# Kernel optimization log

Measured on AMD Instinct MI355X. Metric: run time of the kernel, lower is better.

Reference implementation:

```python
import jax, jax.numpy as jnp
import numpy as np
import math

B, T, F, H = 8, 1024, 512, 8
D = F // H  # 64
MIN_VAL = float(np.finfo(np.float32).min)


def setup_inputs() -> dict:
    key = jax.random.key(0)
    ks = jax.random.split(key, 16)
    w = lambda k, shape: jax.random.normal(k, shape, dtype=jnp.float32) * 0.02
    return {
        "query": jax.random.normal(ks[0], (B, T, F), dtype=jnp.float32),
        "key": jax.random.normal(ks[1], (B, T, F), dtype=jnp.float32),
        "value": jax.random.normal(ks[2], (B, T, F), dtype=jnp.float32),
        "mask": jax.random.randint(ks[3], (B, T, T), 0, 2, dtype=jnp.int32),
        "pos_emb": jax.random.normal(ks[4], (1, T, F), dtype=jnp.float32),
        "Wq": w(ks[5], (F, F)), "bq": jnp.zeros((F,), jnp.float32),
        "Wk": w(ks[6], (F, F)), "bk": jnp.zeros((F,), jnp.float32),
        "Wv": w(ks[7], (F, F)), "bv": jnp.zeros((F,), jnp.float32),
        "Wp": w(ks[8], (F, F)),
        "Wo": w(ks[9], (F, F)), "bo": jnp.zeros((F,), jnp.float32),
        "pos_bias_u": w(ks[10], (H, D)),
        "pos_bias_v": w(ks[11], (H, D)),
    }


def reference(query, key, value, mask, pos_emb, Wq, bq, Wk, bk, Wv, bv, Wp, Wo, bo, pos_bias_u, pos_bias_v):
    n_batch = query.shape[0]
    # projections (torch Linear: x @ W.T + b)
    q = (query @ Wq.T + bq).reshape(n_batch, -1, H, D)          # (B, T1, H, D)
    k = (key @ Wk.T + bk).reshape(n_batch, -1, H, D).transpose(0, 2, 1, 3)    # (B, H, T2, D)
    v = (value @ Wv.T + bv).reshape(n_batch, -1, H, D).transpose(0, 2, 1, 3)  # (B, H, T2, D)
    # relative position projection; pos_emb batch is 1 -> squeeze for broadcast
    p = (pos_emb @ Wp.T).reshape(pos_emb.shape[0], -1, H, D).transpose(0, 2, 1, 3)[0]  # (H, T2, D)

    q_u = q + pos_bias_u  # broadcast (H, D) over (B, T1, H, D)
    q_v = q + pos_bias_v
    matrix_ac = jnp.einsum("bthd,bhsd->bhts", q_u, k)
    matrix_bd = jnp.einsum("bthd,hsd->bhts", q_v, p)
    scores = (matrix_ac + matrix_bd) / math.sqrt(D)  # (B, H, T1, T2)

    m = (mask[:, None, :, :] == 0)  # (B, 1, T1, T2)
    scores = jnp.where(m, MIN_VAL, scores)
    attn = jnp.where(m, 0.0, jax.nn.softmax(scores, axis=-1))

    x = jnp.einsum("bhts,bhsd->bthd", attn, v).reshape(n_batch, -1, H * D)
    return x @ Wo.T + bo
```

## Files before the change

### kernel.cpp

```cpp
#include <hip/hip_runtime.h>

typedef float f32x4 __attribute__((ext_vector_type(4)));
typedef short bf16x8 __attribute__((ext_vector_type(8)));
typedef unsigned short u16x8 __attribute__((ext_vector_type(8)));

__device__ __forceinline__ unsigned short f2bf(float f) {
  union { float f; unsigned int u; } c; c.f = f;
  unsigned int r = (c.u + 0x7fffu + ((c.u >> 16) & 1u)) >> 16;
  return (unsigned short)r;
}
__device__ __forceinline__ float bf2f(unsigned short u) {
  union { unsigned int u; float f; } c; c.u = ((unsigned int)u) << 16;
  return c.f;
}

struct CvtWArgs {
  const float* s[5];
  unsigned short* d[5];
};

__global__ __launch_bounds__(256) void cvt_w(CvtWArgs a) {
  const int seg = blockIdx.y;
  const float* __restrict__ src = a.s[seg];
  unsigned short* __restrict__ dst = a.d[seg];
  int i = (blockIdx.x * 256 + threadIdx.x) * 8;
  float4 v0 = *(const float4*)&src[i];
  float4 v1 = *(const float4*)&src[i + 4];
  u16x8 o;
  o[0] = f2bf(v0.x); o[1] = f2bf(v0.y); o[2] = f2bf(v0.z); o[3] = f2bf(v0.w);
  o[4] = f2bf(v1.x); o[5] = f2bf(v1.y); o[6] = f2bf(v1.z); o[7] = f2bf(v1.w);
  *(u16x8*)&dst[i] = o;
}

__global__ __launch_bounds__(256) void pack_mask(const int* __restrict__ mask,
                                                 unsigned long long* __restrict__ bits) {
  size_t i = (size_t)blockIdx.x * 256 + threadIdx.x;
  unsigned long long b = __ballot(mask[i] != 0);
  if ((threadIdx.x & 63) == 0) bits[i >> 6] = b;
}

template <int IN_FP32, typename OT, int MODE>
__global__ __launch_bounds__(512) void proj_mfma(
    const void* __restrict__ Xv, const unsigned short* __restrict__ W,
    const float* __restrict__ bias, OT* __restrict__ out)
{
  __shared__ unsigned short SM[128 * 64 + 64 * 64];
  unsigned short* AL = SM;
  unsigned short* BL = SM + 128 * 64;
  const int tid = threadIdx.x;
  const int lane = tid & 63, wv = tid >> 6;
  const int lg = lane >> 4, lr = lane & 15;
  const int wm = wv >> 1, wn = wv & 1;
  const int row0 = blockIdx.x * 128, col0 = blockIdx.y * 64;

  f32x4 acc[2][2];
#pragma unroll
  for (int i = 0; i < 2; ++i)
#pragma unroll
    for (int j = 0; j < 2; ++j) { f32x4 z = {0.f,0.f,0.f,0.f}; acc[i][j] = z; }

  for (int k0 = 0; k0 < 512; k0 += 64) {
    __syncthreads();
    if constexpr (IN_FP32) {
      const float* X = (const float*)Xv;
#pragma unroll
      for (int j = 0; j < 2; ++j) {
        int idx = j * 512 + tid;
        int r = idx >> 3, u = idx & 7;
        const float* p = &X[(size_t)(row0 + r) * 512 + k0 + u * 8];
        float4 x0 = *(const float4*)p;
        float4 x1 = *(const float4*)(p + 4);
        u16x8 o;
        o[0] = f2bf(x0.x); o[1] = f2bf(x0.y); o[2] = f2bf(x0.z); o[3] = f2bf(x0.w);
        o[4] = f2bf(x1.x); o[5] = f2bf(x1.y); o[6] = f2bf(x1.z); o[7] = f2bf(x1.w);
        *(u16x8*)&AL[r * 64 + ((u ^ (r & 7)) << 3)] = o;
      }
    } else {
      const unsigned short* X = (const unsigned short*)Xv;
#pragma unroll
      for (int j = 0; j < 2; ++j) {
        int idx = j * 512 + tid;
        int r = idx >> 3, u = idx & 7;
        uint4 v = *(const uint4*)&X[(size_t)(row0 + r) * 512 + k0 + u * 8];
        *(uint4*)&AL[r * 64 + ((u ^ (r & 7)) << 3)] = v;
      }
    }
    {
      int r = tid >> 3, u = tid & 7;
      uint4 w = *(const uint4*)&W[(size_t)(col0 + r) * 512 + k0 + u * 8];
      *(uint4*)&BL[r * 64 + ((u ^ (r & 7)) << 3)] = w;
    }
    __syncthreads();

    bf16x8 af[2][2], bf[2][2];
#pragma unroll
    for (int mf = 0; mf < 2; ++mf)
#pragma unroll
      for (int ks = 0; ks < 2; ++ks) {
        int row = wm * 32 + mf * 16 + lr;
        af[mf][ks] = *(const bf16x8*)&AL[row * 64 + (((ks * 4 + lg) ^ (lr & 7)) << 3)];
      }
#pragma unroll
    for (int nf = 0; nf < 2; ++nf)
#pragma unroll
      for (int ks = 0; ks < 2; ++ks) {
        int col = wn * 32 + nf * 16 + lr;
        bf[nf][ks] = *(const bf16x8*)&BL[col * 64 + (((ks * 4 + lg) ^ (lr & 7)) << 3)];
      }
#pragma unroll
    for (int mf = 0; mf < 2; ++mf)
#pragma unroll
      for (int nf = 0; nf < 2; ++nf)
#pragma unroll
        for (int ks = 0; ks < 2; ++ks)
          acc[mf][nf] = __builtin_amdgcn_mfma_f32_16x16x32_bf16(
              af[mf][ks], bf[nf][ks], acc[mf][nf], 0, 0, 0);
  }

  if constexpr (MODE == 2) {
    unsigned short* TL = SM;
    __syncthreads();
#pragma unroll
    for (int mf = 0; mf < 2; ++mf)
#pragma unroll
      for (int nf = 0; nf < 2; ++nf) {
        int dl = wn * 32 + nf * 16 + lr;
        float bv = bias[col0 + dl];
#pragma unroll
        for (int reg = 0; reg < 4; ++reg) {
          int tl = wm * 32 + mf * 16 + lg * 4 + reg;
          TL[tl * 73 + dl] = f2bf(acc[mf][nf][reg] + bv);
        }
      }
    __syncthreads();
    const int bI = row0 >> 10, hI = col0 >> 6, t0 = row0 & 1023;
#pragma unroll
    for (int j = 0; j < 2; ++j) {
      int slot = j * 512 + tid;
      int d = slot >> 4, ch = slot & 15;
      u16x8 o;
#pragma unroll
      for (int e = 0; e < 8; ++e) o[e] = TL[(ch * 8 + e) * 73 + d];
      *(u16x8*)&out[((size_t)((bI * 8 + hI) * 64) + d) * 1024 + t0 + ch * 8] = o;
    }
  } else {
#pragma unroll
    for (int mf = 0; mf < 2; ++mf)
#pragma unroll
      for (int nf = 0; nf < 2; ++nf) {
        int col = col0 + wn * 32 + nf * 16 + lr;
        float bv = (bias != nullptr) ? bias[col] : 0.f;
#pragma unroll
        for (int reg = 0; reg < 4; ++reg) {
          int n = row0 + wm * 32 + mf * 16 + lg * 4 + reg;
          float val = acc[mf][nf][reg] + bv;
          if (MODE == 0) {
            int bI = n >> 10, t = n & 1023, hI = col >> 6, d = col & 63;
            size_t off = ((size_t)(bI * 8 + hI) * 1024 + t) * 64 + d;
            if constexpr (sizeof(OT) == 2) out[off] = (OT)f2bf(val);
            else out[off] = (OT)val;
          } else {
            out[(size_t)n * 512 + col] = (OT)val;
          }
        }
      }
  }
}

__global__ __launch_bounds__(256) void attn_mfma(
    const unsigned short* __restrict__ Q, const unsigned short* __restrict__ K,
    const unsigned short* __restrict__ P, const unsigned short* __restrict__ Vt,
    const unsigned long long* __restrict__ bits,
    const float* __restrict__ ubias, const float* __restrict__ vbias,
    unsigned short* __restrict__ X)
{
  __shared__ unsigned short KL[64 * 128];
  __shared__ unsigned short VtL[64 * 64];
  __shared__ unsigned short PL[4 * 16 * 72];

  const int tid = threadIdx.x;
  const int lane = tid & 63, wq = tid >> 6;
  const int lg = lane >> 4, lr = lane & 15;
  const int bh = blockIdx.y, b = bh >> 3, h = bh & 7;
  const int tw = blockIdx.x * 64 + wq * 16;

  bf16x8 qa[4];
  {
    const unsigned short* qrow = Q + ((size_t)bh * 1024 + tw + lr) * 64;
    uint4 qlo = *(const uint4*)&qrow[lg * 8];
    uint4 qhi = *(const uint4*)&qrow[32 + lg * 8];
#pragma unroll
    for (int ks = 0; ks < 4; ++ks) {
      int d0 = (ks & 1) * 32 + lg * 8;
      const float* bb = (ks < 2) ? (ubias + h * 64) : (vbias + h * 64);
      float4 b0 = *(const float4*)&bb[d0];
      float4 b1 = *(const float4*)&bb[d0 + 4];
      uint4 qq = (ks & 1) ? qhi : qlo;
      unsigned int qw[4] = {qq.x, qq.y, qq.z, qq.w};
      float bbv[8] = {b0.x, b0.y, b0.z, b0.w, b1.x, b1.y, b1.z, b1.w};
      bf16x8 a;
#pragma unroll
      for (int e = 0; e < 8; ++e) {
        unsigned short qb = (e & 1) ? (unsigned short)(qw[e >> 1] >> 16)
                                    : (unsigned short)(qw[e >> 1] & 0xffffu);
        a[e] = (short)f2bf((bf2f(qb) + bbv[e]) * 0.125f);
      }
      qa[ks] = a;
    }
  }

  f32x4 Ofr[4];
  float m_[4], l_[4];
#pragma unroll
  for (int nf = 0; nf < 4; ++nf) { f32x4 z = {0.f,0.f,0.f,0.f}; Ofr[nf] = z; }
#pragma unroll
  for (int r = 0; r < 4; ++r) { m_[r] = -3.4e38f; l_[r] = 0.f; }

  const unsigned short* Kg = K + (size_t)bh * 65536;
  const unsigned short* Pg = P + (size_t)h * 65536;
  const unsigned short* Vg = Vt + (size_t)bh * 65536;
  const unsigned long long* brow = bits + (size_t)b * 16384;
  unsigned short* Pl = PL + wq * (16 * 72);

  for (int s0t = 0; s0t < 16; ++s0t) {
    const int s0 = s0t * 64;
    __syncthreads();
#pragma unroll
    for (int j = 0; j < 4; ++j) {
      int idx = j * 256 + tid;
      int r = idx >> 4, c = idx & 15;
      uint4 v = (c < 8) ? *(const uint4*)&Kg[(size_t)(s0 + r) * 64 + c * 8]
                        : *(const uint4*)&Pg[(size_t)(s0 + r) * 64 + (c - 8) * 8];
      *(uint4*)&KL[r * 128 + ((c ^ (r & 7)) << 3)] = v;
    }
#pragma unroll
    for (int j = 0; j < 2; ++j) {
      int idx = j * 256 + tid;
      int d = idx >> 3, u = idx & 7;
      uint4 v = *(const uint4*)&Vg[(size_t)d * 1024 + s0 + u * 8];
      *(uint4*)&VtL[d * 64 + ((u ^ (d & 7)) << 3)] = v;
    }
    __syncthreads();

    unsigned long long mw[4];
#pragma unroll
    for (int r = 0; r < 4; ++r)
      mw[r] = brow[(size_t)(tw + lg * 4 + r) * 16 + s0t];

    f32x4 S[4];
#pragma unroll
    for (int nf = 0; nf < 4; ++nf) {
      bf16x8 kb[4];
#pragma unroll
      for (int ks = 0; ks < 4; ++ks)
        kb[ks] = *(const bf16x8*)&KL[(nf * 16 + lr) * 128 + (((ks * 4 + lg) ^ (lr & 7)) << 3)];
      f32x4 a = {0.f, 0.f, 0.f, 0.f};
#pragma unroll
      for (int ks = 0; ks < 4; ++ks)
        a = __builtin_amdgcn_mfma_f32_16x16x32_bf16(qa[ks], kb[ks], a, 0, 0, 0);
      S[nf] = a;
    }

#pragma unroll
    for (int r = 0; r < 4; ++r) {
      float v = fmaxf(fmaxf(S[0][r], S[1][r]), fmaxf(S[2][r], S[3][r]));
      v = fmaxf(v, __shfl_xor(v, 1));
      v = fmaxf(v, __shfl_xor(v, 2));
      v = fmaxf(v, __shfl_xor(v, 4));
      v = fmaxf(v, __shfl_xor(v, 8));
      float mo = m_[r];
      float mn = fmaxf(mo, v);
      m_[r] = mn;
      float sc = __expf(mo - mn);
      l_[r] *= sc;
#pragma unroll
      for (int nf = 0; nf < 4; ++nf) Ofr[nf][r] *= sc;
      float ps = 0.f;
#pragma unroll
      for (int nf = 0; nf < 4; ++nf) {
        float e = __expf(S[nf][r] - mn);
        e = ((mw[r] >> (nf * 16 + lr)) & 1ull) ? e : 0.f;
        S[nf][r] = e;
        ps += e;
      }
      ps += __shfl_xor(ps, 1);
      ps += __shfl_xor(ps, 2);
      ps += __shfl_xor(ps, 4);
      ps += __shfl_xor(ps, 8);
      l_[r] += ps;
    }

#pragma unroll
    for (int nf = 0; nf < 4; ++nf)
#pragma unroll
      for (int r = 0; r < 4; ++r)
        Pl[(lg * 4 + r) * 72 + nf * 16 + lr] = f2bf(S[nf][r]);
    __syncthreads();

    bf16x8 pa[2];
#pragma unroll
    for (int k2 = 0; k2 < 2; ++k2)
      pa[k2] = *(const bf16x8*)&Pl[lr * 72 + k2 * 32 + lg * 8];
#pragma unroll
    for (int nf2 = 0; nf2 < 4; ++nf2) {
      int d = nf2 * 16 + lr;
      bf16x8 vb[2];
#pragma unroll
      for (int k2 = 0; k2 < 2; ++k2)
        vb[k2] = *(const bf16x8*)&VtL[d * 64 + (((k2 * 4 + lg) ^ (d & 7)) << 3)];
#pragma unroll
      for (int k2 = 0; k2 < 2; ++k2)
        Ofr[nf2] = __builtin_amdgcn_mfma_f32_16x16x32_bf16(
            pa[k2], vb[k2], Ofr[nf2], 0, 0, 0);
    }
  }

#pragma unroll
  for (int r = 0; r < 4; ++r) {
    float l = l_[r];
    float inv = (l > 0.f) ? 1.f / l : 0.f;
    int t = tw + lg * 4 + r;
#pragma unroll
    for (int nf2 = 0; nf2 < 4; ++nf2)
      X[((size_t)b * 1024 + t) * 512 + h * 64 + nf2 * 16 + lr] =
          f2bf(Ofr[nf2][r] * inv);
  }
}

extern "C" void kernel_launch(void* const* d_in, const int* in_sizes, int n_in,
                              void* d_out, int out_size, void* d_ws, size_t ws_size,
                              hipStream_t stream) {
  const float* query = (const float*)d_in[0];
  const float* key   = (const float*)d_in[1];
  const float* value = (const float*)d_in[2];
  const int*   mask  = (const int*)d_in[3];
  const float* pos   = (const float*)d_in[4];
  const float* Wq = (const float*)d_in[5];
  const float* bq = (const float*)d_in[6];
  const float* Wk = (const float*)d_in[7];
  const float* bk = (const float*)d_in[8];
  const float* Wv = (const float*)d_in[9];
  const float* bv = (const float*)d_in[10];
  const float* Wp = (const float*)d_in[11];
  const float* Wo = (const float*)d_in[12];
  const float* bo = (const float*)d_in[13];
  const float* ub = (const float*)d_in[14];
  const float* vb = (const float*)d_in[15];
  float* out = (float*)d_out;

  char* w = (char*)d_ws;
  auto alloc = [&](size_t bytes) {
    char* p = w; w += (bytes + 255) & ~(size_t)255; return p;
  };
  const size_t NA = (size_t)8 * 1024 * 512;
  const size_t NW = (size_t)512 * 512;
  const size_t NP = (size_t)1024 * 512;

  unsigned short* wsQ  = (unsigned short*)alloc(NA * 2);
  unsigned short* wsK  = (unsigned short*)alloc(NA * 2);
  unsigned short* wsVt = (unsigned short*)alloc(NA * 2);
  unsigned short* wsP  = (unsigned short*)alloc(NP * 2);
  unsigned short* wsX  = (unsigned short*)alloc(NA * 2);
  unsigned long long* bitsW = (unsigned long long*)alloc((size_t)8 * 1024 * 16 * 8);
  unsigned short* Wqb = (unsigned short*)alloc(NW * 2);
  unsigned short* Wkb = (unsigned short*)alloc(NW * 2);
  unsigned short* Wvb = (unsigned short*)alloc(NW * 2);
  unsigned short* Wpb = (unsigned short*)alloc(NW * 2);
  unsigned short* Wob = (unsigned short*)alloc(NW * 2);

  CvtWArgs ca;
  ca.s[0] = Wq; ca.d[0] = Wqb;
  ca.s[1] = Wk; ca.d[1] = Wkb;
  ca.s[2] = Wv; ca.d[2] = Wvb;
  ca.s[3] = Wp; ca.d[3] = Wpb;
  ca.s[4] = Wo; ca.d[4] = Wob;

  cvt_w<<<dim3(128, 5), dim3(256), 0, stream>>>(ca);
  pack_mask<<<dim3(32768), dim3(256), 0, stream>>>(mask, bitsW);
  proj_mfma<1, unsigned short, 0><<<dim3(64, 8), dim3(512), 0, stream>>>(query, Wqb, bq, wsQ);
  proj_mfma<1, unsigned short, 0><<<dim3(64, 8), dim3(512), 0, stream>>>(key,   Wkb, bk, wsK);
  proj_mfma<1, unsigned short, 2><<<dim3(64, 8), dim3(512), 0, stream>>>(value, Wvb, bv, wsVt);
  proj_mfma<1, unsigned short, 0><<<dim3(8, 8),  dim3(512), 0, stream>>>(pos,   Wpb, nullptr, wsP);
  attn_mfma<<<dim3(16, 64), dim3(256), 0, stream>>>(wsQ, wsK, wsP, wsVt, bitsW, ub, vb, wsX);
  proj_mfma<0, float, 1><<<dim3(64, 8), dim3(512), 0, stream>>>(wsX, Wob, bo, out);
}
```

Measured before the change: 310.3 us.

## Prefetch next tile into registers in projection and attention loops

```diff
diff --git a/kernel.cpp b/kernel.cpp
--- a/kernel.cpp
+++ b/kernel.cpp
@@ -53,44 +53,63 @@
   const int wm = wv >> 1, wn = wv & 1;
   const int row0 = blockIdx.x * 128, col0 = blockIdx.y * 64;
 
+  const int au = tid & 7, ar = tid >> 3;
+
   f32x4 acc[2][2];
 #pragma unroll
   for (int i = 0; i < 2; ++i)
 #pragma unroll
     for (int j = 0; j < 2; ++j) { f32x4 z = {0.f,0.f,0.f,0.f}; acc[i][j] = z; }
 
-  for (int k0 = 0; k0 < 512; k0 += 64) {
-    __syncthreads();
+  float4 a32[2][2];
+  uint4 a16[2];
+  uint4 breg;
+
+  auto proj_issue = [&](int k0) {
     if constexpr (IN_FP32) {
       const float* X = (const float*)Xv;
 #pragma unroll
       for (int j = 0; j < 2; ++j) {
-        int idx = j * 512 + tid;
-        int r = idx >> 3, u = idx & 7;
-        const float* p = &X[(size_t)(row0 + r) * 512 + k0 + u * 8];
-        float4 x0 = *(const float4*)p;
-        float4 x1 = *(const float4*)(p + 4);
-        u16x8 o;
-        o[0] = f2bf(x0.x); o[1] = f2bf(x0.y); o[2] = f2bf(x0.z); o[3] = f2bf(x0.w);
-        o[4] = f2bf(x1.x); o[5] = f2bf(x1.y); o[6] = f2bf(x1.z); o[7] = f2bf(x1.w);
-        *(u16x8*)&AL[r * 64 + ((u ^ (r & 7)) << 3)] = o;
+        const float* p = &X[(size_t)(row0 + ar + 64 * j) * 512 + k0 + au * 8];
+        a32[j][0] = *(const float4*)p;
+        a32[j][1] = *(const float4*)(p + 4);
       }
     } else {
       const unsigned short* X = (const unsigned short*)Xv;
 #pragma unroll
+      for (int j = 0; j < 2; ++j)
+        a16[j] = *(const uint4*)&X[(size_t)(row0 + ar + 64 * j) * 512 + k0 + au * 8];
+    }
+    breg = *(const uint4*)&W[(size_t)(col0 + ar) * 512 + k0 + au * 8];
+  };
+  auto proj_commit = [&]() {
+    if constexpr (IN_FP32) {
+#pragma unroll
       for (int j = 0; j < 2; ++j) {
-        int idx = j * 512 + tid;
-        int r = idx >> 3, u = idx & 7;
-        uint4 v = *(const uint4*)&X[(size_t)(row0 + r) * 512 + k0 + u * 8];
-        *(uint4*)&AL[r * 64 + ((u ^ (r & 7)) << 3)] = v;
-      }
-    }
-    {
-      int r = tid >> 3, u = tid & 7;
-      uint4 w = *(const uint4*)&W[(size_t)(col0 + r) * 512 + k0 + u * 8];
-      *(uint4*)&BL[r * 64 + ((u ^ (r & 7)) << 3)] = w;
-    }
-    __syncthreads();
+        int r = ar + 64 * j;
+        u16x8 o;
+        o[0] = f2bf(a32[j][0].x); o[1] = f2bf(a32[j][0].y);
+        o[2] = f2bf(a32[j][0].z); o[3] = f2bf(a32[j][0].w);
+        o[4] = f2bf(a32[j][1].x); o[5] = f2bf(a32[j][1].y);
+        o[6] = f2bf(a32[j][1].z); o[7] = f2bf(a32[j][1].w);
+        *(u16x8*)&AL[r * 64 + ((au ^ (ar & 7)) << 3)] = o;
+      }
+    } else {
+#pragma unroll
+      for (int j = 0; j < 2; ++j) {
+        int r = ar + 64 * j;
+        *(uint4*)&AL[r * 64 + ((au ^ (ar & 7)) << 3)] = a16[j];
+      }
+    }
+    *(uint4*)&BL[ar * 64 + ((au ^ (ar & 7)) << 3)] = breg;
+  };
+
+  proj_issue(0);
+  proj_commit();
+
+  for (int k0 = 0; k0 < 512; k0 += 64) {
+    __syncthreads();
+    if (k0 < 448) proj_issue(k0 + 64);
 
     bf16x8 af[2][2], bf[2][2];
 #pragma unroll
@@ -115,6 +134,9 @@
         for (int ks = 0; ks < 2; ++ks)
           acc[mf][nf] = __builtin_amdgcn_mfma_f32_16x16x32_bf16(
               af[mf][ks], bf[nf][ks], acc[mf][nf], 0, 0, 0);
+
+    __syncthreads();
+    if (k0 < 448) proj_commit();
   }
 
   if constexpr (MODE == 2) {
@@ -222,25 +244,39 @@
   const unsigned long long* brow = bits + (size_t)b * 16384;
   unsigned short* Pl = PL + wq * (16 * 72);
 
+  const int sc = tid & 15, sr = tid >> 4;
+  const int vu = tid & 7, vd = tid >> 3;
+  const unsigned short* kpsrc = (sc < 8) ? Kg : Pg;
+  const int scc = sc & 7;
+  uint4 kreg[4], vreg[2];
+
+  auto attn_issue = [&](int s0) {
+#pragma unroll
+    for (int j = 0; j < 4; ++j)
+      kreg[j] = *(const uint4*)&kpsrc[(size_t)(s0 + sr + 16 * j) * 64 + scc * 8];
+#pragma unroll
+    for (int j = 0; j < 2; ++j)
+      vreg[j] = *(const uint4*)&Vg[(size_t)(vd + 32 * j) * 1024 + s0 + vu * 8];
+  };
+  auto attn_commit = [&]() {
+#pragma unroll
+    for (int j = 0; j < 4; ++j) {
+      int r = sr + 16 * j;
+      *(uint4*)&KL[r * 128 + ((sc ^ (sr & 7)) << 3)] = kreg[j];
+    }
+#pragma unroll
+    for (int j = 0; j < 2; ++j) {
+      int d = vd + 32 * j;
+      *(uint4*)&VtL[d * 64 + ((vu ^ (vd & 7)) << 3)] = vreg[j];
+    }
+  };
+
+  attn_issue(0);
+  attn_commit();
+
   for (int s0t = 0; s0t < 16; ++s0t) {
-    const int s0 = s0t * 64;
-    __syncthreads();
-#pragma unroll
-    for (int j = 0; j < 4; ++j) {
-      int idx = j * 256 + tid;
-      int r = idx >> 4, c = idx & 15;
-      uint4 v = (c < 8) ? *(const uint4*)&Kg[(size_t)(s0 + r) * 64 + c * 8]
-                        : *(const uint4*)&Pg[(size_t)(s0 + r) * 64 + (c - 8) * 8];
-      *(uint4*)&KL[r * 128 + ((c ^ (r & 7)) << 3)] = v;
-    }
-#pragma unroll
-    for (int j = 0; j < 2; ++j) {
-      int idx = j * 256 + tid;
-      int d = idx >> 3, u = idx & 7;
-      uint4 v = *(const uint4*)&Vg[(size_t)d * 1024 + s0 + u * 8];
-      *(uint4*)&VtL[d * 64 + ((u ^ (d & 7)) << 3)] = v;
-    }
-    __syncthreads();
+    __syncthreads();
+    if (s0t < 15) attn_issue((s0t + 1) * 64);
 
     unsigned long long mw[4];
 #pragma unroll
@@ -271,10 +307,10 @@
       float mo = m_[r];
       float mn = fmaxf(mo, v);
       m_[r] = mn;
-      float sc = __expf(mo - mn);
-      l_[r] *= sc;
-#pragma unroll
-      for (int nf = 0; nf < 4; ++nf) Ofr[nf][r] *= sc;
+      float sc2 = __expf(mo - mn);
+      l_[r] *= sc2;
+#pragma unroll
+      for (int nf = 0; nf < 4; ++nf) Ofr[nf][r] *= sc2;
       float ps = 0.f;
 #pragma unroll
       for (int nf = 0; nf < 4; ++nf) {
@@ -295,7 +331,6 @@
 #pragma unroll
       for (int r = 0; r < 4; ++r)
         Pl[(lg * 4 + r) * 72 + nf * 16 + lr] = f2bf(S[nf][r]);
-    __syncthreads();
 
     bf16x8 pa[2];
 #pragma unroll
@@ -313,6 +348,9 @@
         Ofr[nf2] = __builtin_amdgcn_mfma_f32_16x16x32_bf16(
             pa[k2], vb[k2], Ofr[nf2], 0, 0, 0);
     }
+
+    __syncthreads();
+    if (s0t < 15) attn_commit();
   }
 
 #pragma unroll
```

After: 374.0 us. 20.5% more time.
